# Performance work log

Hardware: AMD Instinct MI355X
Metric: run time of the kernel (lower is better)

## Reference

```python
import jax, jax.numpy as jnp
import numpy as np

K = 9                # snake kernel size
CENTER = K // 2
EXT = 1.0            # extend_scope
EPS = 1e-5           # GroupNorm eps (torch default)


def conv2d(x, w, b, stride, padding):
    out = jax.lax.conv_general_dilated(
        x, w, window_strides=stride, padding=padding,
        dimension_numbers=("NCHW", "OIHW", "NCHW"))
    return out + b[None, :, None, None]


def group_norm(x, gamma, beta, groups):
    B, C, H, W = x.shape
    xg = x.reshape(B, groups, C // groups, H, W)
    mu = xg.mean(axis=(2, 3, 4), keepdims=True)
    var = xg.var(axis=(2, 3, 4), keepdims=True)
    xn = ((xg - mu) / jnp.sqrt(var + EPS)).reshape(B, C, H, W)
    return xn * gamma[None, :, None, None] + beta[None, :, None, None]


def setup_inputs() -> dict:
    key = jax.random.key(0)
    ks = jax.random.split(key, 6)
    B, Cin, Cout, H, W = 4, 64, 64, 128, 128
    x = jax.random.normal(ks[0], (B, Cin, H, W), jnp.float32)
    w_off = jax.random.normal(ks[1], (2 * K, Cin, 3, 3), jnp.float32) * 0.05
    b_off = jax.random.normal(ks[2], (2 * K,), jnp.float32) * 0.01
    g_gn_off = jnp.ones((2 * K,), jnp.float32)
    b_gn_off = jnp.zeros((2 * K,), jnp.float32)
    w_dsc = jax.random.normal(ks[3], (Cout, Cin, K, 1), jnp.float32) * 0.05
    b_dsc = jax.random.normal(ks[4], (Cout,), jnp.float32) * 0.01
    g_gn = jnp.ones((Cout,), jnp.float32)
    b_gn = jnp.zeros((Cout,), jnp.float32)
    return {"x": x, "w_off": w_off, "b_off": b_off,
            "g_gn_off": g_gn_off, "b_gn_off": b_gn_off,
            "w_dsc": w_dsc, "b_dsc": b_dsc, "g_gn": g_gn, "b_gn": b_gn}


def reference(x, w_off, b_off, g_gn_off, b_gn_off, w_dsc, b_dsc, g_gn, b_gn):
    B, Cin, H, W = x.shape
    # offset branch: conv3x3 -> GN(K groups over 2K chans) -> tanh
    off = conv2d(x, w_off, b_off, (1, 1), "SAME")
    off = jnp.tanh(group_norm(off, g_gn_off, b_gn_off, K))
    y_off = off[:, :K]                              # morph=0 uses y offsets, [B,K,H,W]

    # cumulative offsets outward from the kernel center (center entry = 0)
    upper = jnp.cumsum(y_off[:, CENTER + 1:], axis=1)
    lower = jnp.flip(jnp.cumsum(jnp.flip(y_off[:, :CENTER], axis=1), axis=1), axis=1)
    y_off_new = jnp.concatenate(
        [lower, jnp.zeros_like(y_off[:, :1]), upper], axis=1)   # [B,K,H,W]

    # coordinate maps (pixel space)
    y_coord = jnp.arange(H, dtype=x.dtype)[None, None, :, None] + EXT * y_off_new
    x_spread = jnp.linspace(-CENTER, CENTER, K).astype(x.dtype)
    x_coord = jnp.broadcast_to(
        jnp.arange(W, dtype=x.dtype)[None, None, None, :]
        + x_spread[None, :, None, None], y_coord.shape)
    # rearrange b k h w -> b (h k) w
    y_map = y_coord.transpose(0, 2, 1, 3).reshape(B, H * K, W)
    x_map = x_coord.transpose(0, 2, 1, 3).reshape(B, H * K, W)

    # bilinear grid_sample, align_corners=True; clamp-to-range == torch's
    # _coordinate_map_scaling(clamp + [-1,1] normalize) then grid_sample
    yc = jnp.clip(y_map, 0.0, H - 1.0)
    xc = jnp.clip(x_map, 0.0, W - 1.0)
    y0 = jnp.floor(yc); x0 = jnp.floor(xc)
    wy = yc - y0; wx = xc - x0
    y0i = y0.astype(jnp.int32); x0i = x0.astype(jnp.int32)
    y1i = jnp.minimum(y0i + 1, H - 1); x1i = jnp.minimum(x0i + 1, W - 1)

    def samp(f, y0i, y1i, x0i, x1i, wy, wx):
        # f: [C,H,W]; indices/weights: [K*H, W] -> [C, K*H, W]
        v00 = f[:, y0i, x0i]; v01 = f[:, y0i, x1i]
        v10 = f[:, y1i, x0i]; v11 = f[:, y1i, x1i]
        return (v00 * (1 - wy) * (1 - wx) + v01 * (1 - wy) * wx
                + v10 * wy * (1 - wx) + v11 * wy * wx)

    deformed = jax.vmap(samp)(x, y0i, y1i, x0i, x1i, wy, wx)  # [B,C,K*H,W]

    # snake conv: kernel (K,1), stride (K,1), then GN(out//4) + ReLU
    out = conv2d(deformed, w_dsc, b_dsc, (K, 1), "VALID")      # [B,Cout,H,W]
    out = group_norm(out, g_gn, b_gn, w_dsc.shape[0] // 4)
    return jax.nn.relu(out)
```

## Files before the change

### kernel.cpp

```cpp
#include <hip/hip_runtime.h>
#include <hip/hip_bf16.h>
#include <math.h>

#define B 4
#define C 64
#define H 128
#define W 128
#define KK 9
#define CENTER 4
#define HW (H*W)
#define HP 130
#define WP 130

typedef __attribute__((ext_vector_type(8))) short short8;
typedef __attribute__((ext_vector_type(4))) float f4;

#define OFF_OFFT   0
#define OFF_XB     786432
#define OFF_WB     2949632
#define OFF_WOB    2968064
#define OFF_CSUM   2972672
#define OFF_OSUM   2980864

__device__ __forceinline__ unsigned bf16pack(float a, float b) {
    unsigned ua = __builtin_bit_cast(unsigned, a) + 0x8000u;
    unsigned ub = __builtin_bit_cast(unsigned, b) + 0x8000u;
    return __builtin_amdgcn_perm(ub, ua, 0x07060302);
}

__device__ __forceinline__ unsigned lerp_pack(unsigned a, unsigned b, float fw) {
    float alo = __builtin_bit_cast(float, a << 16);
    float ahi = __builtin_bit_cast(float, a & 0xffff0000u);
    float blo = __builtin_bit_cast(float, b << 16);
    float bhi = __builtin_bit_cast(float, b & 0xffff0000u);
    float slo = alo + fw * (blo - alo);
    float shi = ahi + fw * (bhi - ahi);
    return bf16pack(slo, shi);
}

__device__ __forceinline__ float fast_tanh(float x) {
    float e = __expf(2.f * x);
    return 1.f - 2.f * __builtin_amdgcn_rcpf(e + 1.f);
}

__global__ __launch_bounds__(256) void k_prep(const float* __restrict__ x,
                                              const float* __restrict__ w_dsc,
                                              const float* __restrict__ w_off,
                                              unsigned short* __restrict__ xb,
                                              unsigned short* __restrict__ wb,
                                              unsigned short* __restrict__ wob,
                                              float* __restrict__ csum) {
    int bid = blockIdx.x;
    int tid = threadIdx.x;
    if (bid < 512) {
        __shared__ float lt[64 * 129];
        int xcd = bid & 7, i = bid >> 3;
        int hc = i & 15, b = i >> 4;
        int h = (xcd << 4) | hc;
        int ciA = tid >> 2, gA = tid & 3;
        int wlB = tid >> 3, cgB = tid & 7;

        if (tid < 8) {
            *(uint4*)(xb + ((size_t)(b * HP + h + 1) * WP) * 64 + tid * 8)
                = make_uint4(0, 0, 0, 0);
            *(uint4*)(xb + (((size_t)(b * HP + h + 1) * WP) + WP - 1) * 64 + tid * 8)
                = make_uint4(0, 0, 0, 0);
        }
        const float* srcb = x + ((size_t)(b * C + ciA) * HW) + h * W + gA * 8;
        float4 v0[4], v1[4];
#pragma unroll
        for (int c = 0; c < 4; c++) {
            v0[c] = *(const float4*)(srcb + c * 32);
            v1[c] = *(const float4*)(srcb + c * 32 + 4);
        }
#pragma unroll
        for (int c = 0; c < 4; c++) {
            float* d = lt + ciA * 129 + c * 32 + gA * 8;
            d[0] = v0[c].x; d[1] = v0[c].y; d[2] = v0[c].z; d[3] = v0[c].w;
            d[4] = v1[c].x; d[5] = v1[c].y; d[6] = v1[c].z; d[7] = v1[c].w;
        }
        __syncthreads();
#pragma unroll
        for (int c = 0; c < 4; c++) {
            unsigned u[4];
#pragma unroll
            for (int i2 = 0; i2 < 4; i2++) {
                float lo = lt[(cgB * 8 + 2 * i2)     * 129 + c * 32 + wlB];
                float hi = lt[(cgB * 8 + 2 * i2 + 1) * 129 + c * 32 + wlB];
                u[i2] = bf16pack(lo, hi);
            }
            *(uint4*)(xb + ((size_t)((b * HP + h + 1) * WP + c * 32 + wlB + 1)) * 64
                      + cgB * 8) = make_uint4(u[0], u[1], u[2], u[3]);
        }
    } else if (bid < 512 + 8) {
        int r = bid - 512;
        int b = r >> 1, which = r & 1;
        unsigned short* dst = xb + ((size_t)(b * HP + which * (HP - 1)) * WP) * 64;
        for (int t = tid; t < WP * 64 / 8; t += 256)
            *(uint4*)(dst + t * 8) = make_uint4(0, 0, 0, 0);
    } else if (bid < 512 + 8 + 180) {
        int idx = (bid - (512 + 8)) * 256 + tid;
        if (idx < KK * C * C) {
            int k  = idx >> 12;
            int r  = idx & 4095;
            int co = r >> 6;
            int ci = r & 63;
            unsigned u = __builtin_bit_cast(unsigned, w_dsc[(co * C + ci) * KK + k]);
            u = (u + 0x7fffu + ((u >> 16) & 1u)) >> 16;
            wb[idx] = (unsigned short)u;
        } else if (idx < KK * C * C + 9 * 16 * 64) {
            int r   = idx - KK * C * C;
            int tap = r >> 10;
            int j   = (r >> 6) & 15;
            int ci  = r & 63;
            float v = (j < 10) ? w_off[(j * C + ci) * 9 + tap] : 0.f;
            unsigned u = __builtin_bit_cast(unsigned, v);
            u = (u + 0x7fffu + ((u >> 16) & 1u)) >> 16;
            wob[r] = (unsigned short)u;
        }
    } else {
        int z = bid - (512 + 8 + 180);
        int base = z * 1024 + tid * 4;
        *(f4*)(csum + base) = 0;
    }
}

__global__ __launch_bounds__(256, 4) void k_offconv(const unsigned short* __restrict__ xb,
                                                    const unsigned short* __restrict__ wob,
                                                    const float* __restrict__ b_off,
                                                    float* __restrict__ offT,
                                                    float* __restrict__ osum16) {
    __shared__ unsigned short wlds[1152 * 8];
    __shared__ float red[80];
    int bid = blockIdx.x;
    int xcd  = bid & 7;
    int i    = bid >> 3;
    int b    = i >> 5;
    int rest = i & 31;
    int h    = (xcd << 4) | (rest >> 1);
    int half = rest & 1;
    int tid  = threadIdx.x;
    int wid  = tid >> 6;
    int lane = tid & 63;
    int lm = lane & 15, qd = lane >> 4;
    int pw = half * 64 + wid * 16;

    for (int c = tid; c < 1152; c += 256) {
        int row = c >> 3, g = c & 7;
        uint4 v = *(const uint4*)(wob + c * 8);
        int dst = (g ^ (row & 7)) * 144 + row;
        *(uint4*)(wlds + dst * 8) = v;
    }
    __syncthreads();

    f4 acc = 0;
    const unsigned short* xrow = xb + ((size_t)(b * HP + h) * WP) * 64;
    short8 a0_[9], a1_[9];
#pragma unroll
    for (int t = 0; t < 9; t++) {
        int ky = t / 3, kx = t - 3 * (t / 3);
        a0_[t] = *(const short8*)(xrow +
            ((size_t)(ky * WP + pw + lm + kx)) * 64 + qd * 8);
    }
#pragma unroll
    for (int t = 0; t < 9; t++) {
        int ky = t / 3, kx = t - 3 * (t / 3);
        a1_[t] = *(const short8*)(xrow +
            ((size_t)(ky * WP + pw + lm + kx)) * 64 + 32 + qd * 8);
    }
#pragma unroll
    for (int t = 0; t < 9; t++) {
        int row = t * 16 + lm;
        int chunk = ((qd ^ (lm & 7)) * 144) + row;
        short8 w = *(const short8*)(wlds + chunk * 8);
        acc = __builtin_amdgcn_mfma_f32_16x16x32_bf16(a0_[t], w, acc, 0, 0, 0);
    }
#pragma unroll
    for (int t = 0; t < 9; t++) {
        int row = t * 16 + lm;
        int chunk = (((4 + qd) ^ (lm & 7)) * 144) + row;
        short8 w = *(const short8*)(wlds + chunk * 8);
        acc = __builtin_amdgcn_mfma_f32_16x16x32_bf16(a1_[t], w, acc, 0, 0, 0);
    }

    float bo = b_off[lm];
    float sv = 0.f, sq = 0.f;
    int pixbase = (b * H + h) * W;
#pragma unroll
    for (int r = 0; r < 4; r++) {
        float val = acc[r] + bo;
        int p = pw + qd * 4 + r;
        if (lm < 10) {
            offT[(size_t)(pixbase + p) * 12 + lm] = val;
            sv += val; sq += val * val;
        }
    }
    sv += __shfl_xor(sv, 16); sv += __shfl_xor(sv, 32);
    sq += __shfl_xor(sq, 16); sq += __shfl_xor(sq, 32);
    if (lane < 16 && lm < 10) {
        red[(wid * 10 + lm) * 2]     = sv;
        red[(wid * 10 + lm) * 2 + 1] = sq;
    }
    __syncthreads();
    if (tid < 20) {
        int j = tid >> 1, comp = tid & 1;
        float s = red[j * 2 + comp] + red[(10 + j) * 2 + comp] +
                  red[(20 + j) * 2 + comp] + red[(30 + j) * 2 + comp];
        int sidx = (h >> 3) & 15;
        atomicAdd(&osum16[sidx * 40 + b * 10 + (j >> 1) * 2 + comp], s);
    }
}

#define LOADG(GA, GB, K0) do { _Pragma("unroll")                              \
    for (int j = 0; j < 3; j++) {                                             \
        GA[j] = *(const uint4*)(xb + oA[(K0) + j] + so);                      \
        GB[j] = *(const uint4*)(xb + oB[(K0) + j] + so);                      \
    } } while (0)

#define CONSUME(GA, GB, K0) do { _Pragma("unroll")                            \
    for (int j = 0; j < 3; j++) {                                             \
        int k = (K0) + j;                                                     \
        uint4 r;                                                              \
        r.x = lerp_pack(GA[j].x, GB[j].x, fw9[k]);                            \
        r.y = lerp_pack(GA[j].y, GB[j].y, fw9[k]);                            \
        r.z = lerp_pack(GA[j].z, GB[j].z, fw9[k]);                            \
        r.w = lerp_pack(GA[j].w, GB[j].w, fw9[k]);                            \
        short8 afr = __builtin_bit_cast(short8, r);                           \
        _Pragma("unroll")                                                     \
        for (int ct = 0; ct < 4; ct++) {                                      \
            int row = ct * 16 + lm;                                           \
            int chunk = ((qd ^ (lm & 3)) * 576) + k * 64 + row;               \
            short8 bfr = *(const short8*)(wlds + chunk * 8);                  \
            acc[ct] = __builtin_amdgcn_mfma_f32_16x16x32_bf16(afr, bfr,       \
                                                              acc[ct], 0, 0, 0); \
        } } } while (0)

__global__ __launch_bounds__(256, 4) void k_main(const unsigned short* __restrict__ xb,
                                                 const float* __restrict__ offT,
                                                 const float* __restrict__ osum16,
                                                 const float* __restrict__ g_gn_off,
                                                 const float* __restrict__ b_gn_off,
                                                 const unsigned short* __restrict__ wb,
                                                 const float* __restrict__ b_dsc,
                                                 float* __restrict__ outp,
                                                 float* __restrict__ csum16) {
    __shared__ unsigned short wlds[2304 * 8];
    __shared__ float red[512];
    __shared__ float sred[16];

    int bid = blockIdx.x;
    int xcd  = bid & 7;
    int i    = bid >> 3;
    int b    = i >> 5;
    int rest = i & 31;
    int h    = (xcd << 4) | (rest >> 1);
    int p0   = (rest & 1) << 6;
    int tid  = threadIdx.x;
    int wid  = tid >> 6;
    int lane = tid & 63;
    int lm = lane & 15, qd = lane >> 4;

    int ps = p0 + wid * 16 + lm;

    const float* op = offT + (size_t)((b * H + h) * W + ps) * 12;
    f4 o0 = *(const f4*)op;
    f4 o1 = *(const f4*)(op + 4);
    float o8 = op[8];

    if (tid < 160) {
        int gc = tid >> 4, s = tid & 15;
        float v = osum16[s * 40 + b * 10 + gc];
        v += __shfl_xor(v, 1); v += __shfl_xor(v, 2);
        v += __shfl_xor(v, 4); v += __shfl_xor(v, 8);
        if (s == 0) sred[gc] = v;
    }
    for (int c = tid; c < 2304; c += 256) {
        int k = c >> 8, row = (c >> 2) & 63, g2 = c & 3;
        uint4 v = *(const uint4*)(wb + (size_t)k * 4096 + row * 64 + g2 * 8);
        int dst = ((g2 ^ (row & 3)) * 576) + k * 64 + row;
        *(uint4*)(wlds + dst * 8) = v;
    }
    __syncthreads();

    float yoff[KK];
    {
        const float inv_n = 1.f / (2.f * HW);
        float raw[KK] = {o0[0], o0[1], o0[2], o0[3], o1[0], o1[1], o1[2], o1[3], o8};
        float v[KK];
#pragma unroll
        for (int j = 0; j < KK; j++) {
            int g = j >> 1;
            float s  = sred[g * 2];
            float s2 = sred[g * 2 + 1];
            float mean = s * inv_n;
            float var  = s2 * inv_n - mean * mean;
            float rstd = rsqrtf(var + 1e-5f);
            v[j] = fast_tanh((raw[j] - mean) * rstd * g_gn_off[j] + b_gn_off[j]);
        }
        yoff[CENTER] = 0.f;
        float run = 0.f;
#pragma unroll
        for (int k = CENTER - 1; k >= 0; k--) { run += v[k]; yoff[k] = run; }
        run = 0.f;
#pragma unroll
        for (int k = CENTER + 1; k < KK; k++) { run += v[k]; yoff[k] = run; }
    }

    int oA[9], oB[9];
    float fw9[9];
#pragma unroll
    for (int k = 0; k < 9; k++) {
        float yc = fminf(fmaxf((float)h + yoff[k], 0.f), (float)(H - 1));
        float fy = floorf(yc);
        int y0 = (int)fy;
        int dy = (y0 < H - 1) ? (WP * 64) : 0;
        fw9[k] = yc - fy;
        int xi = min(max(ps + k - CENTER, 0), W - 1);
        oA[k] = ((b * HP + y0 + 1) * WP + xi + 1) * 64 + qd * 8;
        oB[k] = oA[k] + dy;
    }

    f4 acc[4];
#pragma unroll
    for (int ct = 0; ct < 4; ct++) acc[ct] = 0;

    {
        const int so = 0;
        uint4 gaA[3], gbA[3], gaB[3], gbB[3];
        LOADG(gaA, gbA, 0);
        LOADG(gaB, gbB, 3);
        CONSUME(gaA, gbA, 0);
        LOADG(gaA, gbA, 6);
        CONSUME(gaB, gbB, 3);
        CONSUME(gaA, gbA, 6);
    }

    __syncthreads();
    for (int c = tid; c < 2304; c += 256) {
        int k = c >> 8, row = (c >> 2) & 63, g2 = c & 3;
        uint4 v = *(const uint4*)(wb + (size_t)k * 4096 + row * 64 + (4 + g2) * 8);
        int dst = ((g2 ^ (row & 3)) * 576) + k * 64 + row;
        *(uint4*)(wlds + dst * 8) = v;
    }
    __syncthreads();

    {
        const int so = 32;
        uint4 gaA[3], gbA[3], gaB[3], gbB[3];
        LOADG(gaA, gbA, 0);
        LOADG(gaB, gbB, 3);
        CONSUME(gaA, gbA, 0);
        LOADG(gaA, gbA, 6);
        CONSUME(gaB, gbB, 3);
        CONSUME(gaA, gbA, 6);
    }

#pragma unroll
    for (int ct = 0; ct < 4; ct++) {
        int co = ct * 16 + lm;
        float bias = b_dsc[co];
        f4 v;
        float sv = 0.f, sq = 0.f;
#pragma unroll
        for (int r = 0; r < 4; r++) {
            v[r] = acc[ct][r] + bias;
            sv += v[r]; sq += v[r] * v[r];
        }
        *(f4*)(outp + ((size_t)(b * C + co)) * HW + h * W + p0 + wid * 16 + qd * 4) = v;
        sv += __shfl_xor(sv, 16); sv += __shfl_xor(sv, 32);
        sq += __shfl_xor(sq, 16); sq += __shfl_xor(sq, 32);
        if (lane < 16) {
            red[((wid * 4 + ct) * 16 + lm) * 2]     = sv;
            red[((wid * 4 + ct) * 16 + lm) * 2 + 1] = sq;
        }
    }
    __syncthreads();
    if (tid < 128) {
        int co = tid >> 1, comp = tid & 1;
        int ct = co >> 4, lmr = co & 15;
        float s = 0.f;
#pragma unroll
        for (int w2 = 0; w2 < 4; w2++)
            s += red[((w2 * 4 + ct) * 16 + lmr) * 2 + comp];
        int sidx = (h >> 3) & 15;
        atomicAdd(&csum16[(sidx * 256 + b * 64 + co) * 2 + comp], s);
    }
}

__global__ __launch_bounds__(256) void k_norm(float* __restrict__ outp,
                                              const float* __restrict__ csum16,
                                              const float* __restrict__ g_gn,
                                              const float* __restrict__ b_gn) {
    __shared__ float lds[2];
    int bid = blockIdx.x;
    int xcd = bid & 7;
    int i   = bid >> 3;
    int b   = i >> 6, co = i & 63;
    int grp = co >> 2;
    int tid = threadIdx.x;

    if (tid < 64) {
        int s = tid >> 2, c = tid & 3;
        const float* p = csum16 + (s * 256 + b * 64 + grp * 4 + c) * 2;
        float v0 = p[0], v1 = p[1];
#pragma unroll
        for (int d = 1; d < 64; d <<= 1) {
            v0 += __shfl_xor(v0, d);
            v1 += __shfl_xor(v1, d);
        }
        if (tid == 0) {
            float n = 4.f * HW;
            float mean = v0 / n;
            float var  = v1 / n - mean * mean;
            float rstd = rsqrtf(var + 1e-5f);
            float sc = rstd * g_gn[co];
            lds[0] = sc;
            lds[1] = b_gn[co] - mean * sc;
        }
    }
    __syncthreads();
    float sc = lds[0], sh = lds[1];

    float4* ptr = (float4*)(outp + ((size_t)(b * C + co)) * HW + xcd * 16 * W);
#pragma unroll
    for (int j = 0; j < 2; j++) {
        float4 vv = ptr[tid + j * 256];
        vv.x = fmaxf(vv.x * sc + sh, 0.f);
        vv.y = fmaxf(vv.y * sc + sh, 0.f);
        vv.z = fmaxf(vv.z * sc + sh, 0.f);
        vv.w = fmaxf(vv.w * sc + sh, 0.f);
        ptr[tid + j * 256] = vv;
    }
}

extern "C" void kernel_launch(void* const* d_in, const int* in_sizes, int n_in,
                              void* d_out, int out_size, void* d_ws, size_t ws_size,
                              hipStream_t stream) {
    const float* x        = (const float*)d_in[0];
    const float* w_off    = (const float*)d_in[1];
    const float* b_off    = (const float*)d_in[2];
    const float* g_gn_off = (const float*)d_in[3];
    const float* b_gn_off = (const float*)d_in[4];
    const float* w_dsc    = (const float*)d_in[5];
    const float* b_dsc    = (const float*)d_in[6];
    const float* g_gn     = (const float*)d_in[7];
    const float* b_gn     = (const float*)d_in[8];
    float* out = (float*)d_out;
    float* ws  = (float*)d_ws;

    float*          offT   = ws + OFF_OFFT;
    unsigned short* xbp    = (unsigned short*)(ws + OFF_XB);
    unsigned short* wbp    = (unsigned short*)(ws + OFF_WB);
    unsigned short* wobp   = (unsigned short*)(ws + OFF_WOB);
    float*          csum16 = ws + OFF_CSUM;
    float*          osum16 = ws + OFF_OSUM;

    k_prep<<<512 + 8 + 180 + 9, 256, 0, stream>>>(x, w_dsc, w_off, xbp, wbp,
                                                  wobp, csum16);
    k_offconv<<<2 * B * H, 256, 0, stream>>>(xbp, wobp, b_off, offT, osum16);
    k_main<<<2 * B * H, 256, 0, stream>>>(xbp, offT, osum16, g_gn_off, b_gn_off,
                                          wbp, b_dsc, out, csum16);
    k_norm<<<2048, 256, 0, stream>>>(out, csum16, g_gn, b_gn);
}
```

Before: 135.7 us.

## Fuse input transpose/bf16 prep into offset conv kernel using LDS tile

Merges the prep kernel and the offset conv kernel into one. Each block loads its three fp32 input rows straight from x, converts them to bf16 into a swizzled LDS tile, writes its centre row out as the unpadded channel-last bf16 copy for the main kernel, and feeds the offset-conv MFMAs from LDS instead of global memory. This drops a kernel launch, the padded buffer with its zeroed borders, and the global round-trip of the intermediate. The GroupNorm partial sums are now written per block with plain stores instead of atomics and reduced in the main kernel. The cost is that neighbouring blocks reload overlapping halo rows, the offset weights are converted redundantly in every block, and occupancy is lower.

```diff
diff --git a/kernel.cpp b/kernel.cpp
--- a/kernel.cpp
+++ b/kernel.cpp
@@ -9,8 +9,7 @@
 #define KK 9
 #define CENTER 4
 #define HW (H*W)
-#define HP 130
-#define WP 130
+#define SWZ(px) (((px) ^ ((px) >> 3)) & 7)
 
 typedef __attribute__((ext_vector_type(8))) short short8;
 typedef __attribute__((ext_vector_type(4))) float f4;
@@ -18,9 +17,8 @@
 #define OFF_OFFT   0
 #define OFF_XB     786432
 #define OFF_WB     2949632
-#define OFF_WOB    2968064
 #define OFF_CSUM   2972672
-#define OFF_OSUM   2980864
+#define OFF_OSUMW  2980864
 
 __device__ __forceinline__ unsigned bf16pack(float a, float b) {
     unsigned ua = __builtin_bit_cast(unsigned, a) + 0x8000u;
@@ -43,144 +41,135 @@
     return 1.f - 2.f * __builtin_amdgcn_rcpf(e + 1.f);
 }
 
-__global__ __launch_bounds__(256) void k_prep(const float* __restrict__ x,
-                                              const float* __restrict__ w_dsc,
-                                              const float* __restrict__ w_off,
-                                              unsigned short* __restrict__ xb,
-                                              unsigned short* __restrict__ wb,
-                                              unsigned short* __restrict__ wob,
-                                              float* __restrict__ csum) {
+__global__ __launch_bounds__(256, 3) void k_offprep(
+        const float* __restrict__ x,
+        const float* __restrict__ w_off,
+        const float* __restrict__ w_dsc,
+        const float* __restrict__ b_off,
+        unsigned short* __restrict__ xb,
+        unsigned short* __restrict__ wb,
+        float* __restrict__ offT,
+        float* __restrict__ osumW,
+        float* __restrict__ csum16) {
     int bid = blockIdx.x;
     int tid = threadIdx.x;
-    if (bid < 512) {
-        __shared__ float lt[64 * 129];
-        int xcd = bid & 7, i = bid >> 3;
-        int hc = i & 15, b = i >> 4;
-        int h = (xcd << 4) | hc;
-        int ciA = tid >> 2, gA = tid & 3;
-        int wlB = tid >> 3, cgB = tid & 7;
-
-        if (tid < 8) {
-            *(uint4*)(xb + ((size_t)(b * HP + h + 1) * WP) * 64 + tid * 8)
-                = make_uint4(0, 0, 0, 0);
-            *(uint4*)(xb + (((size_t)(b * HP + h + 1) * WP) + WP - 1) * 64 + tid * 8)
-                = make_uint4(0, 0, 0, 0);
-        }
-        const float* srcb = x + ((size_t)(b * C + ciA) * HW) + h * W + gA * 8;
-        float4 v0[4], v1[4];
-#pragma unroll
-        for (int c = 0; c < 4; c++) {
-            v0[c] = *(const float4*)(srcb + c * 32);
-            v1[c] = *(const float4*)(srcb + c * 32 + 4);
-        }
-#pragma unroll
-        for (int c = 0; c < 4; c++) {
-            float* d = lt + ciA * 129 + c * 32 + gA * 8;
-            d[0] = v0[c].x; d[1] = v0[c].y; d[2] = v0[c].z; d[3] = v0[c].w;
-            d[4] = v1[c].x; d[5] = v1[c].y; d[6] = v1[c].z; d[7] = v1[c].w;
-        }
-        __syncthreads();
-#pragma unroll
-        for (int c = 0; c < 4; c++) {
-            unsigned u[4];
-#pragma unroll
-            for (int i2 = 0; i2 < 4; i2++) {
-                float lo = lt[(cgB * 8 + 2 * i2)     * 129 + c * 32 + wlB];
-                float hi = lt[(cgB * 8 + 2 * i2 + 1) * 129 + c * 32 + wlB];
-                u[i2] = bf16pack(lo, hi);
-            }
-            *(uint4*)(xb + ((size_t)((b * HP + h + 1) * WP + c * 32 + wlB + 1)) * 64
-                      + cgB * 8) = make_uint4(u[0], u[1], u[2], u[3]);
-        }
-    } else if (bid < 512 + 8) {
-        int r = bid - 512;
-        int b = r >> 1, which = r & 1;
-        unsigned short* dst = xb + ((size_t)(b * HP + which * (HP - 1)) * WP) * 64;
-        for (int t = tid; t < WP * 64 / 8; t += 256)
-            *(uint4*)(dst + t * 8) = make_uint4(0, 0, 0, 0);
-    } else if (bid < 512 + 8 + 180) {
-        int idx = (bid - (512 + 8)) * 256 + tid;
-        if (idx < KK * C * C) {
+
+    if (bid >= 1024) {
+        if (bid < 1024 + 144) {
+            int idx = (bid - 1024) * 256 + tid;
             int k  = idx >> 12;
-            int r  = idx & 4095;
-            int co = r >> 6;
-            int ci = r & 63;
+            int r2 = idx & 4095;
+            int co = r2 >> 6, ci = r2 & 63;
             unsigned u = __builtin_bit_cast(unsigned, w_dsc[(co * C + ci) * KK + k]);
             u = (u + 0x7fffu + ((u >> 16) & 1u)) >> 16;
             wb[idx] = (unsigned short)u;
-        } else if (idx < KK * C * C + 9 * 16 * 64) {
-            int r   = idx - KK * C * C;
-            int tap = r >> 10;
-            int j   = (r >> 6) & 15;
-            int ci  = r & 63;
-            float v = (j < 10) ? w_off[(j * C + ci) * 9 + tap] : 0.f;
-            unsigned u = __builtin_bit_cast(unsigned, v);
-            u = (u + 0x7fffu + ((u >> 16) & 1u)) >> 16;
-            wob[r] = (unsigned short)u;
-        }
-    } else {
-        int z = bid - (512 + 8 + 180);
-        int base = z * 1024 + tid * 4;
-        *(f4*)(csum + base) = 0;
-    }
-}
-
-__global__ __launch_bounds__(256, 4) void k_offconv(const unsigned short* __restrict__ xb,
-                                                    const unsigned short* __restrict__ wob,
-                                                    const float* __restrict__ b_off,
-                                                    float* __restrict__ offT,
-                                                    float* __restrict__ osum16) {
+        } else {
+            int z = bid - (1024 + 144);
+            *(f4*)(csum16 + z * 1024 + tid * 4) = 0;
+        }
+        return;
+    }
+
+    __shared__ unsigned Tt[3 * 66 * 32];
     __shared__ unsigned short wlds[1152 * 8];
     __shared__ float red[80];
-    int bid = blockIdx.x;
+
     int xcd  = bid & 7;
     int i    = bid >> 3;
     int b    = i >> 5;
     int rest = i & 31;
     int h    = (xcd << 4) | (rest >> 1);
     int half = rest & 1;
-    int tid  = threadIdx.x;
     int wid  = tid >> 6;
     int lane = tid & 63;
     int lm = lane & 15, qd = lane >> 4;
-    int pw = half * 64 + wid * 16;
+    int w0 = half * 64;
+    int pw = w0 + wid * 16;
+
+    {
+        int cp = tid >> 3;
+        int gg = tid & 7;
+        int colc = w0 + gg * 8;
+#pragma unroll
+        for (int r = 0; r < 3; r++) {
+            int hr = h - 1 + r;
+            bool vr = ((unsigned)hr < 128u);
+            const float* s0 = x + ((size_t)(b * C + 2 * cp) * HW) + hr * W + colc;
+            float4 a0 = {0,0,0,0}, a1 = {0,0,0,0}, c0 = {0,0,0,0}, c1 = {0,0,0,0};
+            if (vr) {
+                a0 = *(const float4*)s0;       a1 = *(const float4*)(s0 + 4);
+                c0 = *(const float4*)(s0 + HW); c1 = *(const float4*)(s0 + HW + 4);
+            }
+            float va[8] = {a0.x, a0.y, a0.z, a0.w, a1.x, a1.y, a1.z, a1.w};
+            float vc[8] = {c0.x, c0.y, c0.z, c0.w, c1.x, c1.y, c1.z, c1.w};
+#pragma unroll
+            for (int j = 0; j < 8; j++) {
+                int px = 1 + gg * 8 + j;
+                unsigned q = bf16pack(va[j], vc[j]);
+                Tt[(r * 66 + px) * 32 + ((((cp >> 2) ^ SWZ(px)) << 2) | (cp & 3))] = q;
+            }
+        }
+        if (tid < 64) {
+            int ecp = tid & 31, which = tid >> 5;
+            int px = which ? 65 : 0;
+            int col = w0 - 1 + px;
+            bool vc2 = ((unsigned)col < 128u);
+#pragma unroll
+            for (int r = 0; r < 3; r++) {
+                int hr = h - 1 + r;
+                bool v = vc2 && ((unsigned)hr < 128u);
+                float lo = 0.f, hi = 0.f;
+                if (v) {
+                    const float* p = x + ((size_t)(b * C + 2 * ecp) * HW) + hr * W + col;
+                    lo = p[0]; hi = p[HW];
+                }
+                Tt[(r * 66 + px) * 32 + ((((ecp >> 2) ^ SWZ(px)) << 2) | (ecp & 3))]
+                    = bf16pack(lo, hi);
+            }
+        }
+    }
 
     for (int c = tid; c < 1152; c += 256) {
         int row = c >> 3, g = c & 7;
-        uint4 v = *(const uint4*)(wob + c * 8);
+        int tap = row >> 4, j = row & 15;
+        unsigned u[4];
+#pragma unroll
+        for (int i2 = 0; i2 < 4; i2++) {
+            int ci = g * 8 + 2 * i2;
+            float lo = (j < 10) ? w_off[(j * C + ci) * KK + tap]     : 0.f;
+            float hi = (j < 10) ? w_off[(j * C + ci + 1) * KK + tap] : 0.f;
+            u[i2] = bf16pack(lo, hi);
+        }
         int dst = (g ^ (row & 7)) * 144 + row;
-        *(uint4*)(wlds + dst * 8) = v;
-    }
-    __syncthreads();
+        *(uint4*)(wlds + dst * 8) = make_uint4(u[0], u[1], u[2], u[3]);
+    }
+    __syncthreads();
+
+    {
+        int local = 1 + (tid >> 2);
+        int cq = tid & 3;
+        int col = w0 + local - 1;
+        size_t gbase = (((size_t)(b * H + h) * W) + col) * 64 + cq * 16;
+        unsigned i0 = (66 + local) * 32 + (((cq * 2)     ^ SWZ(local)) << 2);
+        unsigned i1 = (66 + local) * 32 + (((cq * 2 + 1) ^ SWZ(local)) << 2);
+        *(uint4*)(xb + gbase)     = *(const uint4*)&Tt[i0];
+        *(uint4*)(xb + gbase + 8) = *(const uint4*)&Tt[i1];
+    }
 
     f4 acc = 0;
-    const unsigned short* xrow = xb + ((size_t)(b * HP + h) * WP) * 64;
-    short8 a0_[9], a1_[9];
-#pragma unroll
-    for (int t = 0; t < 9; t++) {
-        int ky = t / 3, kx = t - 3 * (t / 3);
-        a0_[t] = *(const short8*)(xrow +
-            ((size_t)(ky * WP + pw + lm + kx)) * 64 + qd * 8);
-    }
-#pragma unroll
-    for (int t = 0; t < 9; t++) {
-        int ky = t / 3, kx = t - 3 * (t / 3);
-        a1_[t] = *(const short8*)(xrow +
-            ((size_t)(ky * WP + pw + lm + kx)) * 64 + 32 + qd * 8);
-    }
-#pragma unroll
-    for (int t = 0; t < 9; t++) {
-        int row = t * 16 + lm;
-        int chunk = ((qd ^ (lm & 7)) * 144) + row;
-        short8 w = *(const short8*)(wlds + chunk * 8);
-        acc = __builtin_amdgcn_mfma_f32_16x16x32_bf16(a0_[t], w, acc, 0, 0, 0);
-    }
-#pragma unroll
-    for (int t = 0; t < 9; t++) {
-        int row = t * 16 + lm;
-        int chunk = (((4 + qd) ^ (lm & 7)) * 144) + row;
-        short8 w = *(const short8*)(wlds + chunk * 8);
-        acc = __builtin_amdgcn_mfma_f32_16x16x32_bf16(a1_[t], w, acc, 0, 0, 0);
+#pragma unroll
+    for (int s = 0; s < 2; s++) {
+#pragma unroll
+        for (int t = 0; t < 9; t++) {
+            int ky = t / 3, kx = t - 3 * (t / 3);
+            int px = wid * 16 + lm + kx;
+            unsigned aidx = (ky * 66 + px) * 32 + (((s * 4 + qd) ^ SWZ(px)) << 2);
+            short8 afr = *(const short8*)((const unsigned short*)&Tt[aidx]);
+            int row = t * 16 + lm;
+            int chunk = (((s * 4 + qd) ^ (lm & 7)) * 144) + row;
+            short8 w = *(const short8*)(wlds + chunk * 8);
+            acc = __builtin_amdgcn_mfma_f32_16x16x32_bf16(afr, w, acc, 0, 0, 0);
+        }
     }
 
     float bo = b_off[lm];
@@ -206,8 +195,11 @@
         int j = tid >> 1, comp = tid & 1;
         float s = red[j * 2 + comp] + red[(10 + j) * 2 + comp] +
                   red[(20 + j) * 2 + comp] + red[(30 + j) * 2 + comp];
-        int sidx = (h >> 3) & 15;
-        atomicAdd(&osum16[sidx * 40 + b * 10 + (j >> 1) * 2 + comp], s);
+        float sg = s + __shfl_xor(s, 2);
+        if ((tid & 2) == 0) {
+            int slot = b * 256 + h * 2 + half;
+            osumW[(size_t)slot * 10 + (tid >> 2) * 2 + comp] = sg;
+        }
     }
 }
 
@@ -237,7 +229,7 @@
 
 __global__ __launch_bounds__(256, 4) void k_main(const unsigned short* __restrict__ xb,
                                                  const float* __restrict__ offT,
-                                                 const float* __restrict__ osum16,
+                                                 const float* __restrict__ osumW,
                                                  const float* __restrict__ g_gn_off,
                                                  const float* __restrict__ b_gn_off,
                                                  const unsigned short* __restrict__ wb,
@@ -246,7 +238,7 @@
                                                  float* __restrict__ csum16) {
     __shared__ unsigned short wlds[2304 * 8];
     __shared__ float red[512];
-    __shared__ float sred[16];
+    __shared__ float wred[4][10];
 
     int bid = blockIdx.x;
     int xcd  = bid & 7;
@@ -267,12 +259,21 @@
     f4 o1 = *(const f4*)(op + 4);
     float o8 = op[8];
 
-    if (tid < 160) {
-        int gc = tid >> 4, s = tid & 15;
-        float v = osum16[s * 40 + b * 10 + gc];
-        v += __shfl_xor(v, 1); v += __shfl_xor(v, 2);
-        v += __shfl_xor(v, 4); v += __shfl_xor(v, 8);
-        if (s == 0) sred[gc] = v;
+    {
+        const float* p = osumW + (size_t)(b * 256 + wid * 64 + lane) * 10;
+        float v[10];
+#pragma unroll
+        for (int j = 0; j < 10; j++) v[j] = p[j];
+#pragma unroll
+        for (int j = 0; j < 10; j++) {
+            v[j] += __shfl_xor(v[j], 1);  v[j] += __shfl_xor(v[j], 2);
+            v[j] += __shfl_xor(v[j], 4);  v[j] += __shfl_xor(v[j], 8);
+            v[j] += __shfl_xor(v[j], 16); v[j] += __shfl_xor(v[j], 32);
+        }
+        if (lane == 0) {
+#pragma unroll
+            for (int j = 0; j < 10; j++) wred[wid][j] = v[j];
+        }
     }
     for (int c = tid; c < 2304; c += 256) {
         int k = c >> 8, row = (c >> 2) & 63, g2 = c & 3;
@@ -290,8 +291,10 @@
 #pragma unroll
         for (int j = 0; j < KK; j++) {
             int g = j >> 1;
-            float s  = sred[g * 2];
-            float s2 = sred[g * 2 + 1];
+            float s  = wred[0][g * 2] + wred[1][g * 2] +
+                       wred[2][g * 2] + wred[3][g * 2];
+            float s2 = wred[0][g * 2 + 1] + wred[1][g * 2 + 1] +
+                       wred[2][g * 2 + 1] + wred[3][g * 2 + 1];
             float mean = s * inv_n;
             float var  = s2 * inv_n - mean * mean;
             float rstd = rsqrtf(var + 1e-5f);
@@ -313,10 +316,10 @@
         float yc = fminf(fmaxf((float)h + yoff[k], 0.f), (float)(H - 1));
         float fy = floorf(yc);
         int y0 = (int)fy;
-        int dy = (y0 < H - 1) ? (WP * 64) : 0;
+        int dy = (y0 < H - 1) ? (W * 64) : 0;
         fw9[k] = yc - fy;
         int xi = min(max(ps + k - CENTER, 0), W - 1);
-        oA[k] = ((b * HP + y0 + 1) * WP + xi + 1) * 64 + qd * 8;
+        oA[k] = ((b * H + y0) * W + xi) * 64 + qd * 8;
         oB[k] = oA[k] + dy;
     }
 
@@ -451,14 +454,12 @@
     float*          offT   = ws + OFF_OFFT;
     unsigned short* xbp    = (unsigned short*)(ws + OFF_XB);
     unsigned short* wbp    = (unsigned short*)(ws + OFF_WB);
-    unsigned short* wobp   = (unsigned short*)(ws + OFF_WOB);
     float*          csum16 = ws + OFF_CSUM;
-    float*          osum16 = ws + OFF_OSUM;
-
-    k_prep<<<512 + 8 + 180 + 9, 256, 0, stream>>>(x, w_dsc, w_off, xbp, wbp,
-                                                  wobp, csum16);
-    k_offconv<<<2 * B * H, 256, 0, stream>>>(xbp, wobp, b_off, offT, osum16);
-    k_main<<<2 * B * H, 256, 0, stream>>>(xbp, offT, osum16, g_gn_off, b_gn_off,
+    float*          osumW  = ws + OFF_OSUMW;
+
+    k_offprep<<<1024 + 144 + 8, 256, 0, stream>>>(x, w_off, w_dsc, b_off,
+                                                  xbp, wbp, offT, osumW, csum16);
+    k_main<<<2 * B * H, 256, 0, stream>>>(xbp, offT, osumW, g_gn_off, b_gn_off,
                                           wbp, b_dsc, out, csum16);
     k_norm<<<2048, 256, 0, stream>>>(out, csum16, g_gn, b_gn);
 }
```

After: 139.9 us. +3.1%, slower.
